# Kernel tuning notes

Measured on AMD Instinct MI355X. Metric: run time of the kernel, lower is better.

## Reference

```python
import jax, jax.numpy as jnp
import numpy as np

EMBED_DIM = 512
NUM_HEADS = 8
HEAD_DIM = EMBED_DIM // NUM_HEADS
NUM_TEXTS = 512
NUM_VIDS = 512
NUM_FRAMES = 12


def setup_inputs() -> dict:
    key = jax.random.key(0)
    ks = jax.random.split(key, 10)
    s = 1.0 / np.sqrt(EMBED_DIM)
    return {
        "text_embeds": jax.random.normal(ks[0], (NUM_TEXTS, EMBED_DIM), jnp.float32),
        "video_embeds": jax.random.normal(ks[1], (NUM_VIDS, NUM_FRAMES, EMBED_DIM), jnp.float32),
        "Wq": jax.random.normal(ks[2], (EMBED_DIM, EMBED_DIM), jnp.float32) * s,
        "bq": jax.random.normal(ks[3], (EMBED_DIM,), jnp.float32) * s,
        "Wk": jax.random.normal(ks[4], (EMBED_DIM, EMBED_DIM), jnp.float32) * s,
        "bk": jax.random.normal(ks[5], (EMBED_DIM,), jnp.float32) * s,
        "Wv": jax.random.normal(ks[6], (EMBED_DIM, EMBED_DIM), jnp.float32) * s,
        "bv": jax.random.normal(ks[7], (EMBED_DIM,), jnp.float32) * s,
        "Wo": jax.random.normal(ks[8], (EMBED_DIM, EMBED_DIM), jnp.float32) * s,
        "bo": jax.random.normal(ks[9], (EMBED_DIM,), jnp.float32) * s,
    }


def reference(text_embeds, video_embeds, Wq, bq, Wk, bk, Wv, bv, Wo, bo):
    T = text_embeds.shape[0]
    V, F, D = video_embeds.shape
    H, Hd = NUM_HEADS, HEAD_DIM

    # q: [T, D] -> [T, H, Hd]
    q = (text_embeds @ Wq + bq).reshape(T, H, Hd)
    # k, v: [V, F, D] -> [V, F, H, Hd]
    k = (video_embeds @ Wk + bk).reshape(V, F, H, Hd)
    v = (video_embeds @ Wv + bv).reshape(V, F, H, Hd)

    # shared-query broadcast logits: [V, H, F, T]
    logits = jnp.einsum("vfhd,thd->vhft", k, q) / np.sqrt(Hd).astype(jnp.float32)
    # softmax over frames (dim F)
    weights = jax.nn.softmax(logits, axis=2)

    # weighted sum over frames: [V, H, Hd, T] -> [V, T, D]
    attn = jnp.einsum("vfhd,vhft->vthd", v, weights).reshape(V, T, D)
    return attn @ Wo + bo
```

## Files before the change

### kernel.cpp

```cpp
#include <hip/hip_runtime.h>
#include <stdint.h>

#define T_  512
#define V_  512
#define F_  12
#define FP_ 16
#define D_  512
#define H_  8
#define HF_ 96

using half8  = __attribute__((ext_vector_type(8))) _Float16;
using f32x4  = __attribute__((ext_vector_type(4))) float;
using uint4v = __attribute__((ext_vector_type(4))) unsigned int;

#define OFF_TB   (0L)
#define OFF_VB   (524288L)
#define OFF_WQT  (OFF_VB  + 8388608L)
#define OFF_WKT  (OFF_WQT + 524288L)
#define OFF_WVT  (OFF_WKT + 524288L)
#define OFF_WOT  (OFF_WVT + 524288L)
#define OFF_QB   (OFF_WOT + 524288L)
#define OFF_KP   (OFF_QB  + 524288L)
#define OFF_VP   (OFF_KP  + 8388608L)
#define OFF_ZT   (OFF_VP  + 8388608L)
#define OFF_WT   (OFF_ZT  + 50331648L)

__device__ __forceinline__ unsigned short f2h(float x) {
  _Float16 h = (_Float16)x;
  return __builtin_bit_cast(unsigned short, h);
}

__device__ __forceinline__ void cvt8_store(float4 a, float4 b, unsigned short* dst) {
  unsigned int w0 = f2h(a.x) | ((unsigned int)f2h(a.y) << 16);
  unsigned int w1 = f2h(a.z) | ((unsigned int)f2h(a.w) << 16);
  unsigned int w2 = f2h(b.x) | ((unsigned int)f2h(b.y) << 16);
  unsigned int w3 = f2h(b.z) | ((unsigned int)f2h(b.w) << 16);
  uint4v v = {w0, w1, w2, w3};
  *(uint4v*)dst = v;
}

__global__ __launch_bounds__(256) void k0_prep(
    const float* __restrict__ text, const float* __restrict__ video,
    const float* __restrict__ Wq, const float* __restrict__ Wk,
    const float* __restrict__ Wv, const float* __restrict__ Wo, char* ws) {
  __shared__ unsigned short tl[64][72];
  int bx = blockIdx.x, tid = threadIdx.x;
  if (bx < 128) {
    unsigned short* tb = (unsigned short*)(ws + OFF_TB);
    long i = ((long)bx * 256 + tid) * 8;
    float4 a = *(const float4*)(text + i);
    float4 b = *(const float4*)(text + i + 4);
    cvt8_store(a, b, tb + i);
  } else if (bx < 2176) {
    unsigned short* vb = (unsigned short*)(ws + OFF_VB);
    long j = ((long)(bx - 128) * 256 + tid) * 8;
    int row = (int)(j >> 9);
    int c   = (int)(j & 511);
    int f = row & 15, v = row >> 4;
    if (f < F_) {
      const float* src = video + ((long)(v * F_ + f) << 9) + c;
      float4 a = *(const float4*)src;
      float4 b = *(const float4*)(src + 4);
      cvt8_store(a, b, vb + j);
    } else {
      uint4v z = {0, 0, 0, 0};
      *(uint4v*)(vb + j) = z;
    }
  } else {
    int tix = bx - 2176;
    int w = tix >> 6, tile = tix & 63;
    const float* W = (w == 0) ? Wq : (w == 1) ? Wk : (w == 2) ? Wv : Wo;
    unsigned short* WT = (unsigned short*)(ws +
        ((w == 0) ? OFF_WQT : (w == 1) ? OFF_WKT : (w == 2) ? OFF_WVT : OFF_WOT));
    int r0 = (tile >> 3) * 64, c0 = (tile & 7) * 64;
    int rr = tid >> 4, cc = (tid & 15) * 4;
#pragma unroll
    for (int j2 = 0; j2 < 4; ++j2) {
      int r = rr + j2 * 16;
      float4 a = *(const float4*)(W + (long)(r0 + r) * 512 + c0 + cc);
      tl[cc + 0][r] = f2h(a.x);
      tl[cc + 1][r] = f2h(a.y);
      tl[cc + 2][r] = f2h(a.z);
      tl[cc + 3][r] = f2h(a.w);
    }
    __syncthreads();
    int row_l = tid >> 2, u = (tid & 3) * 16;
    uint4v x0 = *(uint4v*)&tl[row_l][u];
    uint4v x1 = *(uint4v*)&tl[row_l][u + 8];
    unsigned short* dst = WT + (long)(c0 + row_l) * 512 + r0 + u;
    *(uint4v*)dst = x0;
    *(uint4v*)(dst + 8) = x1;
  }
}

__global__ __launch_bounds__(256) void k1_proj(
    char* ws, const float* __restrict__ bq, const float* __restrict__ bk,
    const float* __restrict__ bv) {
  __shared__ unsigned short As[128 * 72];
  __shared__ unsigned short Bs[128 * 72];
  int bx = blockIdx.x, tid = threadIdx.x;
  int nt = bx & 3, mt = bx >> 2;
  const unsigned short* A;
  const unsigned short* BT;
  const float* bias;
  float scale;
  unsigned short* out;
  int m0;
  if (mt < 4) {
    A = (const unsigned short*)(ws + OFF_TB);
    BT = (const unsigned short*)(ws + OFF_WQT);
    bias = bq; scale = 0.125f;
    out = (unsigned short*)(ws + OFF_QB);
    m0 = mt << 7;
  } else if (mt < 68) {
    A = (const unsigned short*)(ws + OFF_VB);
    BT = (const unsigned short*)(ws + OFF_WKT);
    bias = bk; scale = 1.0f;
    out = (unsigned short*)(ws + OFF_KP);
    m0 = (mt - 4) << 7;
  } else {
    A = (const unsigned short*)(ws + OFF_VB);
    BT = (const unsigned short*)(ws + OFF_WVT);
    bias = bv; scale = 1.0f;
    out = (unsigned short*)(ws + OFF_VP);
    m0 = (mt - 68) << 7;
  }
  int n0 = nt << 7;
  int lane = tid & 63, wid = tid >> 6;
  int mw = (wid >> 1) << 6, nw = (wid & 1) << 6;
  int l15 = lane & 15, g = lane >> 4;
  f32x4 acc[4][4];
#pragma unroll
  for (int i = 0; i < 4; i++)
#pragma unroll
    for (int j = 0; j < 4; j++) acc[i][j] = (f32x4){0.f, 0.f, 0.f, 0.f};

  for (int ks = 0; ks < 8; ++ks) {
    __syncthreads();
#pragma unroll
    for (int j = 0; j < 4; ++j) {
      int flat = (j * 256 + tid) * 8;
      int row = flat >> 6, col = flat & 63;
      uint4v va = *(const uint4v*)(A + (long)(m0 + row) * 512 + ks * 64 + col);
      uint4v vb = *(const uint4v*)(BT + (long)(n0 + row) * 512 + ks * 64 + col);
      *(uint4v*)(As + row * 72 + col) = va;
      *(uint4v*)(Bs + row * 72 + col) = vb;
    }
    __syncthreads();
#pragma unroll
    for (int k2 = 0; k2 < 2; ++k2) {
      half8 a[4], b[4];
#pragma unroll
      for (int i = 0; i < 4; i++) {
        a[i] = *(const half8*)(As + (mw + i * 16 + l15) * 72 + k2 * 32 + (g << 3));
        b[i] = *(const half8*)(Bs + (nw + i * 16 + l15) * 72 + k2 * 32 + (g << 3));
      }
#pragma unroll
      for (int i = 0; i < 4; i++)
#pragma unroll
        for (int j = 0; j < 4; j++)
          acc[i][j] = __builtin_amdgcn_mfma_f32_16x16x32_f16(a[i], b[j], acc[i][j], 0, 0, 0);
    }
  }
#pragma unroll
  for (int j = 0; j < 4; j++) {
    int n = n0 + nw + j * 16 + l15;
    float bsv = bias[n];
#pragma unroll
    for (int i = 0; i < 4; i++) {
      int rbase = m0 + mw + i * 16 + (g << 2);
#pragma unroll
      for (int r = 0; r < 4; r++) {
        float x = (acc[i][j][r] + bsv) * scale;
        out[(long)(rbase + r) * 512 + n] = f2h(x);
      }
    }
  }
}

__global__ __launch_bounds__(256) void k2_z(char* ws) {
  int bx = blockIdx.x, tid = threadIdx.x;
  int v = bx >> 2, nt = bx & 3;
  const unsigned short* WoT = (const unsigned short*)(ws + OFF_WOT);
  const unsigned short* vp = (const unsigned short*)(ws + OFF_VP);
  unsigned short* Zt = (unsigned short*)(ws + OFF_ZT);
  int lane = tid & 63, wid = tid >> 6;
  int f = lane & 15, g = lane >> 4;
  int nb = (nt << 7) + (wid << 5);
  const unsigned short* vpv = vp + ((long)(v * 16 + f) << 9);
  for (int h = 0; h < H_; ++h) {
    half8 b0 = *(const half8*)(vpv + h * 64 + (g << 3));
    half8 b1 = *(const half8*)(vpv + h * 64 + 32 + (g << 3));
#pragma unroll
    for (int mf = 0; mf < 2; ++mf) {
      int n = nb + (mf << 4) + f;
      half8 a0 = *(const half8*)(WoT + ((long)n << 9) + h * 64 + (g << 3));
      half8 a1 = *(const half8*)(WoT + ((long)n << 9) + h * 64 + 32 + (g << 3));
      f32x4 acc = {0.f, 0.f, 0.f, 0.f};
      acc = __builtin_amdgcn_mfma_f32_16x16x32_f16(a0, b0, acc, 0, 0, 0);
      acc = __builtin_amdgcn_mfma_f32_16x16x32_f16(a1, b1, acc, 0, 0, 0);
      if (f < F_) {
#pragma unroll
        for (int r = 0; r < 4; ++r) {
          int nr = nb + (mf << 4) + (g << 2) + r;
          Zt[(long)(v * 512 + nr) * 96 + h * 12 + f] = f2h(acc[r]);
        }
      }
    }
  }
}

__global__ __launch_bounds__(256) void k3_w(char* ws) {
  __shared__ unsigned short Ks[16 * 520];
  int bx = blockIdx.x, tid = threadIdx.x;
  int v = bx >> 3, tt = bx & 7;
  const unsigned short* qb = (const unsigned short*)(ws + OFF_QB);
  const unsigned short* kp = (const unsigned short*)(ws + OFF_KP);
  unsigned short* Wt = (unsigned short*)(ws + OFF_WT);
  const unsigned short* kpv = kp + ((long)v << 13);
#pragma unroll
  for (int j = 0; j < 4; ++j) {
    int flat = (j * 256 + tid) * 8;
    int row = flat >> 9, col = flat & 511;
    uint4v x = *(const uint4v*)(kpv + flat);
    *(uint4v*)(Ks + row * 520 + col) = x;
  }
  __syncthreads();
  int lane = tid & 63, wid = tid >> 6;
  int f = lane & 15, g = lane >> 4;
  int t0 = (tt << 6) + (wid << 4);
  const unsigned short* qrow = qb + ((long)(t0 + f) << 9);
  for (int h = 0; h < H_; ++h) {
    half8 a0 = *(const half8*)(qrow + h * 64 + (g << 3));
    half8 a1 = *(const half8*)(qrow + h * 64 + 32 + (g << 3));
    half8 b0 = *(const half8*)(Ks + f * 520 + h * 64 + (g << 3));
    half8 b1 = *(const half8*)(Ks + f * 520 + h * 64 + 32 + (g << 3));
    f32x4 acc = {0.f, 0.f, 0.f, 0.f};
    acc = __builtin_amdgcn_mfma_f32_16x16x32_f16(a0, b0, acc, 0, 0, 0);
    acc = __builtin_amdgcn_mfma_f32_16x16x32_f16(a1, b1, acc, 0, 0, 0);
#pragma unroll
    for (int r = 0; r < 4; ++r) {
      float x = (f < F_) ? acc[r] : -1e30f;
      float mm = x;
      mm = fmaxf(mm, __shfl_xor(mm, 1, 16));
      mm = fmaxf(mm, __shfl_xor(mm, 2, 16));
      mm = fmaxf(mm, __shfl_xor(mm, 4, 16));
      mm = fmaxf(mm, __shfl_xor(mm, 8, 16));
      float e = (f < F_) ? __expf(x - mm) : 0.0f;
      float ss = e;
      ss += __shfl_xor(ss, 1, 16);
      ss += __shfl_xor(ss, 2, 16);
      ss += __shfl_xor(ss, 4, 16);
      ss += __shfl_xor(ss, 8, 16);
      if (f < F_) {
        int t = t0 + (g << 2) + r;
        Wt[(long)(v * 512 + t) * 96 + h * 12 + f] = f2h(e / ss);
      }
    }
  }
}

__global__ __launch_bounds__(256) void k4_out(char* ws, const float* __restrict__ bo,
                                              float* __restrict__ outp) {
  __shared__ unsigned short As[128 * 104];
  __shared__ unsigned short Bs[128 * 104];
  int bx = blockIdx.x, tid = threadIdx.x;
  int v = bx >> 4, tt = (bx >> 2) & 3, nt = bx & 3;
  const unsigned short* Wt = (const unsigned short*)(ws + OFF_WT);
  const unsigned short* Zt = (const unsigned short*)(ws + OFF_ZT);
  const unsigned short* Asrc = Wt + ((long)v * 512 + tt * 128) * 96;
  const unsigned short* Bsrc = Zt + ((long)v * 512 + nt * 128) * 96;
#pragma unroll
  for (int j = 0; j < 6; ++j) {
    int flat = (j * 256 + tid) * 8;
    int row = flat / 96;
    int col = flat - row * 96;
    uint4v a = *(const uint4v*)(Asrc + flat);
    uint4v b = *(const uint4v*)(Bsrc + flat);
    *(uint4v*)(As + row * 104 + col) = a;
    *(uint4v*)(Bs + row * 104 + col) = b;
  }
  __syncthreads();
  int lane = tid & 63, wid = tid >> 6;
  int g = lane >> 4, l15 = lane & 15;
  int mw = (wid >> 1) << 6, nw = (wid & 1) << 6;
  f32x4 acc[4][4];
#pragma unroll
  for (int i = 0; i < 4; i++)
#pragma unroll
    for (int j = 0; j < 4; j++) acc[i][j] = (f32x4){0.f, 0.f, 0.f, 0.f};
#pragma unroll
  for (int ks = 0; ks < 3; ++ks) {
    half8 a[4], b[4];
#pragma unroll
    for (int i = 0; i < 4; i++) {
      a[i] = *(const half8*)(As + (mw + i * 16 + l15) * 104 + ks * 32 + (g << 3));
      b[i] = *(const half8*)(Bs + (nw + i * 16 + l15) * 104 + ks * 32 + (g << 3));
    }
#pragma unroll
    for (int i = 0; i < 4; i++)
#pragma unroll
      for (int j = 0; j < 4; j++)
        acc[i][j] = __builtin_amdgcn_mfma_f32_16x16x32_f16(a[i], b[j], acc[i][j], 0, 0, 0);
  }
#pragma unroll
  for (int j = 0; j < 4; j++) {
    int n = (nt << 7) + nw + j * 16 + l15;
    float bias = bo[n];
#pragma unroll
    for (int i = 0; i < 4; i++) {
      long tb_ = (long)(v * 512 + (tt << 7) + mw + i * 16 + (g << 2));
#pragma unroll
      for (int r = 0; r < 4; r++) {
        outp[(tb_ + r) * 512 + n] = acc[i][j][r] + bias;
      }
    }
  }
}

extern "C" void kernel_launch(void* const* d_in, const int* in_sizes, int n_in,
                              void* d_out, int out_size, void* d_ws, size_t ws_size,
                              hipStream_t stream) {
  const float* text  = (const float*)d_in[0];
  const float* video = (const float*)d_in[1];
  const float* Wq = (const float*)d_in[2];
  const float* bq = (const float*)d_in[3];
  const float* Wk = (const float*)d_in[4];
  const float* bk = (const float*)d_in[5];
  const float* Wv = (const float*)d_in[6];
  const float* bv = (const float*)d_in[7];
  const float* Wo = (const float*)d_in[8];
  const float* bo = (const float*)d_in[9];
  char* ws = (char*)d_ws;
  float* out = (float*)d_out;

  k0_prep<<<dim3(2432), dim3(256), 0, stream>>>(text, video, Wq, Wk, Wv, Wo, ws);
  k1_proj<<<dim3(528), dim3(256), 0, stream>>>(ws, bq, bk, bv);
  k2_z<<<dim3(2048), dim3(256), 0, stream>>>(ws);
  k3_w<<<dim3(4096), dim3(256), 0, stream>>>(ws);
  k4_out<<<dim3(8192), dim3(256), 0, stream>>>(ws, bo, out);
}
```

Baseline: 753.2 us.

## Fuse logits-softmax, V·Wo projection and output GEMM into one kernel

Replaces the three kernels k2_z, k3_w and k4_out with a single k5_fused kernel. Each block computes its softmax weights from Q·K and its Z = V·Wo tile directly into LDS, then runs the output GEMM. This removes the large Zt/Wt workspace write and re-read and two launches. The cost is that each weight tile and each Z tile is recomputed by four blocks. The softmax also drops the max subtraction, which risks overflow if logits grow large. A block-index swizzle is added to group blocks that share data.

```diff
diff --git a/kernel.cpp b/kernel.cpp
--- a/kernel.cpp
+++ b/kernel.cpp
@@ -12,6 +12,7 @@
 using half8  = __attribute__((ext_vector_type(8))) _Float16;
 using f32x4  = __attribute__((ext_vector_type(4))) float;
 using uint4v = __attribute__((ext_vector_type(4))) unsigned int;
+using uint2v = __attribute__((ext_vector_type(2))) unsigned int;
 
 #define OFF_TB   (0L)
 #define OFF_VB   (524288L)
@@ -22,8 +23,6 @@
 #define OFF_QB   (OFF_WOT + 524288L)
 #define OFF_KP   (OFF_QB  + 524288L)
 #define OFF_VP   (OFF_KP  + 8388608L)
-#define OFF_ZT   (OFF_VP  + 8388608L)
-#define OFF_WT   (OFF_ZT  + 50331648L)
 
 __device__ __forceinline__ unsigned short f2h(float x) {
   _Float16 h = (_Float16)x;
@@ -178,111 +177,82 @@
   }
 }
 
-__global__ __launch_bounds__(256) void k2_z(char* ws) {
-  int bx = blockIdx.x, tid = threadIdx.x;
-  int v = bx >> 2, nt = bx & 3;
-  const unsigned short* WoT = (const unsigned short*)(ws + OFF_WOT);
-  const unsigned short* vp = (const unsigned short*)(ws + OFF_VP);
-  unsigned short* Zt = (unsigned short*)(ws + OFF_ZT);
-  int lane = tid & 63, wid = tid >> 6;
-  int f = lane & 15, g = lane >> 4;
-  int nb = (nt << 7) + (wid << 5);
-  const unsigned short* vpv = vp + ((long)(v * 16 + f) << 9);
-  for (int h = 0; h < H_; ++h) {
-    half8 b0 = *(const half8*)(vpv + h * 64 + (g << 3));
-    half8 b1 = *(const half8*)(vpv + h * 64 + 32 + (g << 3));
-#pragma unroll
-    for (int mf = 0; mf < 2; ++mf) {
-      int n = nb + (mf << 4) + f;
-      half8 a0 = *(const half8*)(WoT + ((long)n << 9) + h * 64 + (g << 3));
-      half8 a1 = *(const half8*)(WoT + ((long)n << 9) + h * 64 + 32 + (g << 3));
-      f32x4 acc = {0.f, 0.f, 0.f, 0.f};
-      acc = __builtin_amdgcn_mfma_f32_16x16x32_f16(a0, b0, acc, 0, 0, 0);
-      acc = __builtin_amdgcn_mfma_f32_16x16x32_f16(a1, b1, acc, 0, 0, 0);
-      if (f < F_) {
-#pragma unroll
-        for (int r = 0; r < 4; ++r) {
-          int nr = nb + (mf << 4) + (g << 2) + r;
-          Zt[(long)(v * 512 + nr) * 96 + h * 12 + f] = f2h(acc[r]);
-        }
-      }
-    }
-  }
-}
-
-__global__ __launch_bounds__(256) void k3_w(char* ws) {
-  __shared__ unsigned short Ks[16 * 520];
-  int bx = blockIdx.x, tid = threadIdx.x;
-  int v = bx >> 3, tt = bx & 7;
-  const unsigned short* qb = (const unsigned short*)(ws + OFF_QB);
-  const unsigned short* kp = (const unsigned short*)(ws + OFF_KP);
-  unsigned short* Wt = (unsigned short*)(ws + OFF_WT);
-  const unsigned short* kpv = kp + ((long)v << 13);
-#pragma unroll
-  for (int j = 0; j < 4; ++j) {
-    int flat = (j * 256 + tid) * 8;
-    int row = flat >> 9, col = flat & 511;
-    uint4v x = *(const uint4v*)(kpv + flat);
-    *(uint4v*)(Ks + row * 520 + col) = x;
-  }
-  __syncthreads();
-  int lane = tid & 63, wid = tid >> 6;
-  int f = lane & 15, g = lane >> 4;
-  int t0 = (tt << 6) + (wid << 4);
-  const unsigned short* qrow = qb + ((long)(t0 + f) << 9);
-  for (int h = 0; h < H_; ++h) {
-    half8 a0 = *(const half8*)(qrow + h * 64 + (g << 3));
-    half8 a1 = *(const half8*)(qrow + h * 64 + 32 + (g << 3));
-    half8 b0 = *(const half8*)(Ks + f * 520 + h * 64 + (g << 3));
-    half8 b1 = *(const half8*)(Ks + f * 520 + h * 64 + 32 + (g << 3));
-    f32x4 acc = {0.f, 0.f, 0.f, 0.f};
-    acc = __builtin_amdgcn_mfma_f32_16x16x32_f16(a0, b0, acc, 0, 0, 0);
-    acc = __builtin_amdgcn_mfma_f32_16x16x32_f16(a1, b1, acc, 0, 0, 0);
-#pragma unroll
-    for (int r = 0; r < 4; ++r) {
-      float x = (f < F_) ? acc[r] : -1e30f;
-      float mm = x;
-      mm = fmaxf(mm, __shfl_xor(mm, 1, 16));
-      mm = fmaxf(mm, __shfl_xor(mm, 2, 16));
-      mm = fmaxf(mm, __shfl_xor(mm, 4, 16));
-      mm = fmaxf(mm, __shfl_xor(mm, 8, 16));
-      float e = (f < F_) ? __expf(x - mm) : 0.0f;
-      float ss = e;
-      ss += __shfl_xor(ss, 1, 16);
-      ss += __shfl_xor(ss, 2, 16);
-      ss += __shfl_xor(ss, 4, 16);
-      ss += __shfl_xor(ss, 8, 16);
-      if (f < F_) {
-        int t = t0 + (g << 2) + r;
-        Wt[(long)(v * 512 + t) * 96 + h * 12 + f] = f2h(e / ss);
-      }
-    }
-  }
-}
-
-__global__ __launch_bounds__(256) void k4_out(char* ws, const float* __restrict__ bo,
-                                              float* __restrict__ outp) {
+__global__ __launch_bounds__(256) void k5_fused(char* ws, const float* __restrict__ bo,
+                                                float* __restrict__ outp) {
   __shared__ unsigned short As[128 * 104];
   __shared__ unsigned short Bs[128 * 104];
   int bx = blockIdx.x, tid = threadIdx.x;
-  int v = bx >> 4, tt = (bx >> 2) & 3, nt = bx & 3;
-  const unsigned short* Wt = (const unsigned short*)(ws + OFF_WT);
-  const unsigned short* Zt = (const unsigned short*)(ws + OFF_ZT);
-  const unsigned short* Asrc = Wt + ((long)v * 512 + tt * 128) * 96;
-  const unsigned short* Bsrc = Zt + ((long)v * 512 + nt * 128) * 96;
-#pragma unroll
-  for (int j = 0; j < 6; ++j) {
-    int flat = (j * 256 + tid) * 8;
-    int row = flat / 96;
-    int col = flat - row * 96;
-    uint4v a = *(const uint4v*)(Asrc + flat);
-    uint4v b = *(const uint4v*)(Bsrc + flat);
-    *(uint4v*)(As + row * 104 + col) = a;
-    *(uint4v*)(Bs + row * 104 + col) = b;
-  }
+  int bsw = (bx & 7) * 1024 + (bx >> 3);
+  int v = bsw >> 4, tt = (bsw >> 2) & 3, nt = bsw & 3;
+
+  const unsigned short* QB = (const unsigned short*)(ws + OFF_QB);
+  const unsigned short* KP = (const unsigned short*)(ws + OFF_KP);
+  const unsigned short* VP = (const unsigned short*)(ws + OFF_VP);
+  const unsigned short* WOT = (const unsigned short*)(ws + OFF_WOT);
+
+  int lane = tid & 63, wid = tid >> 6;
+  int l15 = lane & 15, g = lane >> 4;
+
+  {
+    const unsigned short* kpr = KP + ((long)(v * 16 + l15) << 9);
+#pragma unroll
+    for (int h = 0; h < H_; ++h) {
+      half8 a0 = *(const half8*)(kpr + h * 64 + (g << 3));
+      half8 a1 = *(const half8*)(kpr + h * 64 + 32 + (g << 3));
+#pragma unroll
+      for (int ti = 0; ti < 2; ++ti) {
+        int tl = (wid << 5) + (ti << 4);
+        const unsigned short* qr = QB + ((long)(tt * 128 + tl + l15) << 9);
+        half8 b0 = *(const half8*)(qr + h * 64 + (g << 3));
+        half8 b1 = *(const half8*)(qr + h * 64 + 32 + (g << 3));
+        f32x4 acc = {0.f, 0.f, 0.f, 0.f};
+        acc = __builtin_amdgcn_mfma_f32_16x16x32_f16(a0, b0, acc, 0, 0, 0);
+        acc = __builtin_amdgcn_mfma_f32_16x16x32_f16(a1, b1, acc, 0, 0, 0);
+        float e0 = (g < 3) ? __expf(acc[0]) : 0.f;
+        float e1 = (g < 3) ? __expf(acc[1]) : 0.f;
+        float e2 = (g < 3) ? __expf(acc[2]) : 0.f;
+        float e3 = (g < 3) ? __expf(acc[3]) : 0.f;
+        float s = e0 + e1 + e2 + e3;
+        s += __shfl_xor(s, 16);
+        s += __shfl_xor(s, 32);
+        float inv = 1.0f / s;
+        if (g < 3) {
+          unsigned int w0 = f2h(e0 * inv) | ((unsigned int)f2h(e1 * inv) << 16);
+          unsigned int w1 = f2h(e2 * inv) | ((unsigned int)f2h(e3 * inv) << 16);
+          uint2v pk = {w0, w1};
+          *(uint2v*)(As + (tl + l15) * 104 + h * 12 + (g << 2)) = pk;
+        }
+      }
+    }
+  }
+
+  {
+    const unsigned short* vpr = VP + ((long)(v * 16 + l15) << 9);
+#pragma unroll
+    for (int h = 0; h < H_; ++h) {
+      half8 a0 = *(const half8*)(vpr + h * 64 + (g << 3));
+      half8 a1 = *(const half8*)(vpr + h * 64 + 32 + (g << 3));
+#pragma unroll
+      for (int mf = 0; mf < 2; ++mf) {
+        int nl = (wid << 5) + (mf << 4);
+        const unsigned short* wor = WOT + ((long)(nt * 128 + nl + l15) << 9);
+        half8 b0 = *(const half8*)(wor + h * 64 + (g << 3));
+        half8 b1 = *(const half8*)(wor + h * 64 + 32 + (g << 3));
+        f32x4 acc = {0.f, 0.f, 0.f, 0.f};
+        acc = __builtin_amdgcn_mfma_f32_16x16x32_f16(a0, b0, acc, 0, 0, 0);
+        acc = __builtin_amdgcn_mfma_f32_16x16x32_f16(a1, b1, acc, 0, 0, 0);
+        if (g < 3) {
+          unsigned int w0 = f2h(acc[0]) | ((unsigned int)f2h(acc[1]) << 16);
+          unsigned int w1 = f2h(acc[2]) | ((unsigned int)f2h(acc[3]) << 16);
+          uint2v pk = {w0, w1};
+          *(uint2v*)(Bs + (nl + l15) * 104 + h * 12 + (g << 2)) = pk;
+        }
+      }
+    }
+  }
+
   __syncthreads();
-  int lane = tid & 63, wid = tid >> 6;
-  int g = lane >> 4, l15 = lane & 15;
+
   int mw = (wid >> 1) << 6, nw = (wid & 1) << 6;
   f32x4 acc[4][4];
 #pragma unroll
@@ -336,7 +306,5 @@
 
   k0_prep<<<dim3(2432), dim3(256), 0, stream>>>(text, video, Wq, Wk, Wv, Wo, ws);
   k1_proj<<<dim3(528), dim3(256), 0, stream>>>(ws, bq, bk, bv);
-  k2_z<<<dim3(2048), dim3(256), 0, stream>>>(ws);
-  k3_w<<<dim3(4096), dim3(256), 0, stream>>>(ws);
-  k4_out<<<dim3(8192), dim3(256), 0, stream>>>(ws, bo, out);
-}
+  k5_fused<<<dim3(8192), dim3(256), 0, stream>>>(ws, bo, out);
+}
```

Result: slower. 882.7 us (+17.2%).
